# Kernel tuning notes

Measured on AMD Instinct MI355X. Metric: run time of the kernel, lower is better.

The kernel has to match this reference:

```python
import jax, jax.numpy as jnp
import numpy as np

NUM_ENT = 100000
DIM = 768
BATCH = 4096
TAU = 0.05
ALPHA = 0.5
LARGE_NUM = 1e9


def setup_inputs() -> dict:
    key = jax.random.key(0)
    k1, k2 = jax.random.split(key)
    emb = jax.random.normal(k1, (NUM_ENT, DIM), dtype=jnp.float32)
    train_links = jax.random.randint(k2, (BATCH, 2), 0, NUM_ENT, dtype=jnp.int64)
    return {"emb": emb, "train_links": train_links}


def _soft_xent(logits, batch_size):
    # target is one-hot on column i for row i -> pick diagonal of log_softmax
    logprobs = jax.nn.log_softmax(logits, axis=1)
    diag = logprobs[jnp.arange(batch_size), jnp.arange(batch_size)]
    return -jnp.sum(diag) / batch_size


def reference(emb, train_links):
    # L2-normalize embeddings (norm=True default)
    emb_n = emb / jnp.linalg.norm(emb, axis=1, keepdims=True)
    h1 = emb_n[train_links[:, 0]]  # [B, D]
    h2 = emb_n[train_links[:, 1]]  # [B, D]
    B = h1.shape[0]
    mask = jnp.eye(B, dtype=h1.dtype) * LARGE_NUM

    logits_aa = jnp.matmul(h1, h1.T) / TAU - mask  # [B, B]
    logits_bb = jnp.matmul(h2, h2.T) / TAU - mask
    logits_ab = jnp.matmul(h1, h2.T) / TAU
    logits_ba = jnp.matmul(h2, h1.T) / TAU

    logits_a = jnp.concatenate([logits_ab, logits_aa], axis=1)  # [B, 2B]
    logits_b = jnp.concatenate([logits_ba, logits_bb], axis=1)

    loss_a = _soft_xent(logits_a, B)
    loss_b = _soft_xent(logits_b, B)
    return ALPHA * loss_a + (1.0 - ALPHA) * loss_b
```

## Files before the change

### kernel.cpp

```cpp
#include <hip/hip_runtime.h>
#include <hip/hip_bf16.h>
#include <math.h>

#define NUM_ENT 100000
#define DIM 768
#define BATCH 4096
#define INV_TAU 20.0f
#define QSCALE 16.0f
#define LOGIT_SCALE (INV_TAU / (QSCALE * QSCALE))

typedef __attribute__((ext_vector_type(4))) float f32x4;

__global__ __launch_bounds__(256) void gather_norm(
    const float* __restrict__ emb, const int* __restrict__ links,
    unsigned char* __restrict__ hn1, unsigned char* __restrict__ hn2)
{
    const int t    = threadIdx.x;
    const int wave = t >> 6;
    const int lane = t & 63;
    const int rowId = blockIdx.x * 4 + wave;
    const int b     = rowId >> 1;
    const int which = rowId & 1;
    const int src   = links[2 * b + which];
    const float* srcRow = emb + (size_t)src * DIM;

    float4 v0 = ((const float4*)srcRow)[lane];
    float4 v1 = ((const float4*)srcRow)[lane + 64];
    float4 v2 = ((const float4*)srcRow)[lane + 128];

    float ss = v0.x * v0.x + v0.y * v0.y + v0.z * v0.z + v0.w * v0.w
             + v1.x * v1.x + v1.y * v1.y + v1.z * v1.z + v1.w * v1.w
             + v2.x * v2.x + v2.y * v2.y + v2.z * v2.z + v2.w * v2.w;
    #pragma unroll
    for (int off = 32; off >= 1; off >>= 1) ss += __shfl_xor(ss, off);
    const float scale = rsqrtf(ss) * QSCALE;

    unsigned char* dst = (which ? hn2 : hn1) + (size_t)b * DIM;
    int p0 = __builtin_amdgcn_cvt_pk_fp8_f32(v0.x * scale, v0.y * scale, 0, false);
    p0     = __builtin_amdgcn_cvt_pk_fp8_f32(v0.z * scale, v0.w * scale, p0, true);
    int p1 = __builtin_amdgcn_cvt_pk_fp8_f32(v1.x * scale, v1.y * scale, 0, false);
    p1     = __builtin_amdgcn_cvt_pk_fp8_f32(v1.z * scale, v1.w * scale, p1, true);
    int p2 = __builtin_amdgcn_cvt_pk_fp8_f32(v2.x * scale, v2.y * scale, 0, false);
    p2     = __builtin_amdgcn_cvt_pk_fp8_f32(v2.z * scale, v2.w * scale, p2, true);
    ((unsigned int*)dst)[lane]       = (unsigned int)p0;
    ((unsigned int*)dst)[lane + 64]  = (unsigned int)p1;
    ((unsigned int*)dst)[lane + 128] = (unsigned int)p2;
}

__global__ __launch_bounds__(256) void gram_sym(
    const unsigned char* __restrict__ hn1, const unsigned char* __restrict__ hn2,
    float* __restrict__ S, float* __restrict__ diag)
{
    const int ct = blockIdx.x;
    const int rt = blockIdx.y;
    const int matId = blockIdx.z;
    if (matId > 0 && ct < rt) return;

    const unsigned char* A  = (matId == 2) ? hn2 : hn1;
    const unsigned char* Bm = (matId == 1) ? hn1 : hn2;
    const int  rowTarget = (matId == 2) ? 1 : 0;
    const int  colTarget = (matId == 1) ? 0 : 1;
    const bool maskDiag  = (matId > 0) && (rt == ct);
    const bool doColsum  = (matId == 0) || (rt != ct);
    const bool captureDiag = (matId == 0);

    __shared__ unsigned char sA[128 * 32];
    __shared__ unsigned char sB[128 * 32];

    const int t    = threadIdx.x;
    const int lane = t & 63;
    const int wave = t >> 6;
    const int wm   = wave >> 1, wn = wave & 1;
    const int quad = lane >> 4, l16 = lane & 15;
    const int row0 = rt * 128;
    const int col0 = ct * 128;

    f32x4 acc[4][4];
    #pragma unroll
    for (int im = 0; im < 4; ++im)
        #pragma unroll
        for (int jn = 0; jn < 4; ++jn)
            acc[im][jn] = (f32x4){0.f, 0.f, 0.f, 0.f};

    for (int kk = 0; kk < DIM; kk += 32) {
        {
            int r = t >> 1, h = t & 1;
            int koff = ((h + ((r >> 2) & 1)) & 1) * 16;
            const unsigned char* ga = A  + (size_t)(row0 + r) * DIM + kk + koff;
            const unsigned char* gb = Bm + (size_t)(col0 + r) * DIM + kk + koff;
            __builtin_amdgcn_global_load_lds(
                (const __attribute__((address_space(1))) void*)ga,
                (__attribute__((address_space(3))) void*)(sA + t * 16), 16, 0, 0);
            __builtin_amdgcn_global_load_lds(
                (const __attribute__((address_space(1))) void*)gb,
                (__attribute__((address_space(3))) void*)(sB + t * 16), 16, 0, 0);
        }
        __syncthreads();

        long long af[4], bfr[4];
        const int hk = quad >> 1, q8 = (quad & 1) * 8;
        #pragma unroll
        for (int im = 0; im < 4; ++im) {
            int row = wm * 64 + im * 16 + l16;
            int hl  = (hk + ((row >> 2) & 1)) & 1;
            af[im] = *(const long long*)&sA[row * 32 + hl * 16 + q8];
        }
        #pragma unroll
        for (int jn = 0; jn < 4; ++jn) {
            int row = wn * 64 + jn * 16 + l16;
            int hl  = (hk + ((row >> 2) & 1)) & 1;
            bfr[jn] = *(const long long*)&sB[row * 32 + hl * 16 + q8];
        }

        #pragma unroll
        for (int im = 0; im < 4; ++im)
            #pragma unroll
            for (int jn = 0; jn < 4; ++jn)
                acc[im][jn] = __builtin_amdgcn_mfma_f32_16x16x32_fp8_fp8(
                    af[im], bfr[jn], acc[im][jn], 0, 0, 0);
        __syncthreads();
    }

    float csum[4] = {0.f, 0.f, 0.f, 0.f};
    #pragma unroll
    for (int im = 0; im < 4; ++im) {
        #pragma unroll
        for (int r = 0; r < 4; ++r) {
            const int gi = row0 + wm * 64 + im * 16 + quad * 4 + r;
            float rsum = 0.f;
            #pragma unroll
            for (int jn = 0; jn < 4; ++jn) {
                const int gj = col0 + wn * 64 + jn * 16 + l16;
                float logit = acc[im][jn][r] * LOGIT_SCALE;
                bool isDiag = (gi == gj);
                if (captureDiag && isDiag) diag[gi] = logit;
                float e = __expf(logit);
                if (maskDiag && isDiag) e = 0.f;
                rsum += e;
                csum[jn] += e;
            }
            rsum += __shfl_xor(rsum, 1);
            rsum += __shfl_xor(rsum, 2);
            rsum += __shfl_xor(rsum, 4);
            rsum += __shfl_xor(rsum, 8);
            if (l16 == 0) atomicAdd(&S[rowTarget * BATCH + gi], rsum);
        }
    }
    if (doColsum) {
        #pragma unroll
        for (int jn = 0; jn < 4; ++jn) {
            float c = csum[jn];
            c += __shfl_xor(c, 16);
            c += __shfl_xor(c, 32);
            if (quad == 0) {
                const int gj = col0 + wn * 64 + jn * 16 + l16;
                atomicAdd(&S[colTarget * BATCH + gj], c);
            }
        }
    }
}

__global__ __launch_bounds__(1024) void finalize(
    const float* __restrict__ S, const float* __restrict__ diag,
    float* __restrict__ out)
{
    int t = threadIdx.x;
    float local = 0.f;
    for (int i = t; i < BATCH; i += 1024) {
        float lse_a = logf(S[i]);
        float lse_b = logf(S[BATCH + i]);
        local += 0.5f * (lse_a + lse_b) - diag[i];
    }
    #pragma unroll
    for (int off = 32; off >= 1; off >>= 1) local += __shfl_xor(local, off);
    __shared__ float wsum[16];
    if ((t & 63) == 0) wsum[t >> 6] = local;
    __syncthreads();
    if (t == 0) {
        float tot = 0.f;
        #pragma unroll
        for (int w = 0; w < 16; ++w) tot += wsum[w];
        out[0] = tot / (float)BATCH;
    }
}

extern "C" void kernel_launch(void* const* d_in, const int* in_sizes, int n_in,
                              void* d_out, int out_size, void* d_ws, size_t ws_size,
                              hipStream_t stream)
{
    const float* emb  = (const float*)d_in[0];
    const int* links  = (const int*)d_in[1];

    char* ws = (char*)d_ws;
    unsigned char* hn1 = (unsigned char*)ws;
    unsigned char* hn2 = (unsigned char*)(ws + (size_t)BATCH * DIM);
    float* S    = (float*)(ws + (size_t)BATCH * DIM * 2);
    float* diag = (float*)(ws + (size_t)BATCH * DIM * 2 + 2 * BATCH * 4);

    hipMemsetAsync(S, 0, 2 * BATCH * sizeof(float), stream);

    gather_norm<<<dim3(2 * BATCH / 4), 256, 0, stream>>>(emb, links, hn1, hn2);
    gram_sym<<<dim3(32, 32, 3), 256, 0, stream>>>(hn1, hn2, S, diag);
    finalize<<<1, 1024, 0, stream>>>(S, diag, (float*)d_out);
}
```

Baseline: 426.1 us.

## Switch Gram GEMM from fp8 to int8 MFMA with 64-wide K tiles

Quantizes the normalized embeddings to int8 with scale 256 instead of fp8, and uses the 16x16x64 i8 MFMA with a 64-byte K tile and a new LDS swizzle. This halves the number of K iterations and barriers and gives better mantissa precision than fp8. It also folds the S memset into the gather kernel to drop a separate launch. Int8 clamping at 127 is safe for unit-norm rows scaled by 256 only because per-element magnitudes are small, which risks clipping outliers.

```diff
diff --git a/kernel.cpp b/kernel.cpp
--- a/kernel.cpp
+++ b/kernel.cpp
@@ -6,18 +6,30 @@
 #define DIM 768
 #define BATCH 4096
 #define INV_TAU 20.0f
-#define QSCALE 16.0f
+#define QSCALE 256.0f
 #define LOGIT_SCALE (INV_TAU / (QSCALE * QSCALE))
 
-typedef __attribute__((ext_vector_type(4))) float f32x4;
+typedef __attribute__((ext_vector_type(4))) int i32x4;
+
+__device__ inline unsigned int pack_i8x4(float a, float b, float c, float d) {
+    int ia = __float2int_rn(fminf(fmaxf(a, -127.f), 127.f));
+    int ib = __float2int_rn(fminf(fmaxf(b, -127.f), 127.f));
+    int ic = __float2int_rn(fminf(fmaxf(c, -127.f), 127.f));
+    int id = __float2int_rn(fminf(fmaxf(d, -127.f), 127.f));
+    return (unsigned int)((ia & 0xff) | ((ib & 0xff) << 8) |
+                          ((ic & 0xff) << 16) | ((id & 0xff) << 24));
+}
 
 __global__ __launch_bounds__(256) void gather_norm(
     const float* __restrict__ emb, const int* __restrict__ links,
-    unsigned char* __restrict__ hn1, unsigned char* __restrict__ hn2)
+    unsigned char* __restrict__ hn1, unsigned char* __restrict__ hn2,
+    float* __restrict__ S)
 {
     const int t    = threadIdx.x;
     const int wave = t >> 6;
     const int lane = t & 63;
+    if (blockIdx.x < 32) S[blockIdx.x * 256 + t] = 0.f;
+
     const int rowId = blockIdx.x * 4 + wave;
     const int b     = rowId >> 1;
     const int which = rowId & 1;
@@ -36,15 +48,12 @@
     const float scale = rsqrtf(ss) * QSCALE;
 
     unsigned char* dst = (which ? hn2 : hn1) + (size_t)b * DIM;
-    int p0 = __builtin_amdgcn_cvt_pk_fp8_f32(v0.x * scale, v0.y * scale, 0, false);
-    p0     = __builtin_amdgcn_cvt_pk_fp8_f32(v0.z * scale, v0.w * scale, p0, true);
-    int p1 = __builtin_amdgcn_cvt_pk_fp8_f32(v1.x * scale, v1.y * scale, 0, false);
-    p1     = __builtin_amdgcn_cvt_pk_fp8_f32(v1.z * scale, v1.w * scale, p1, true);
-    int p2 = __builtin_amdgcn_cvt_pk_fp8_f32(v2.x * scale, v2.y * scale, 0, false);
-    p2     = __builtin_amdgcn_cvt_pk_fp8_f32(v2.z * scale, v2.w * scale, p2, true);
-    ((unsigned int*)dst)[lane]       = (unsigned int)p0;
-    ((unsigned int*)dst)[lane + 64]  = (unsigned int)p1;
-    ((unsigned int*)dst)[lane + 128] = (unsigned int)p2;
+    ((unsigned int*)dst)[lane] =
+        pack_i8x4(v0.x * scale, v0.y * scale, v0.z * scale, v0.w * scale);
+    ((unsigned int*)dst)[lane + 64] =
+        pack_i8x4(v1.x * scale, v1.y * scale, v1.z * scale, v1.w * scale);
+    ((unsigned int*)dst)[lane + 128] =
+        pack_i8x4(v2.x * scale, v2.y * scale, v2.z * scale, v2.w * scale);
 }
 
 __global__ __launch_bounds__(256) void gram_sym(
@@ -64,8 +73,8 @@
     const bool doColsum  = (matId == 0) || (rt != ct);
     const bool captureDiag = (matId == 0);
 
-    __shared__ unsigned char sA[128 * 32];
-    __shared__ unsigned char sB[128 * 32];
+    __shared__ unsigned char sA[128 * 64];
+    __shared__ unsigned char sB[128 * 64];
 
     const int t    = threadIdx.x;
     const int lane = t & 63;
@@ -75,48 +84,52 @@
     const int row0 = rt * 128;
     const int col0 = ct * 128;
 
-    f32x4 acc[4][4];
+    i32x4 acc[4][4];
     #pragma unroll
     for (int im = 0; im < 4; ++im)
         #pragma unroll
         for (int jn = 0; jn < 4; ++jn)
-            acc[im][jn] = (f32x4){0.f, 0.f, 0.f, 0.f};
-
-    for (int kk = 0; kk < DIM; kk += 32) {
-        {
-            int r = t >> 1, h = t & 1;
-            int koff = ((h + ((r >> 2) & 1)) & 1) * 16;
-            const unsigned char* ga = A  + (size_t)(row0 + r) * DIM + kk + koff;
-            const unsigned char* gb = Bm + (size_t)(col0 + r) * DIM + kk + koff;
+            acc[im][jn] = (i32x4){0, 0, 0, 0};
+
+    for (int kk = 0; kk < DIM; kk += 64) {
+        #pragma unroll
+        for (int rd = 0; rd < 2; ++rd) {
+            const int idx = rd * 256 + t;
+            const int r   = idx >> 2;
+            const int p   = idx & 3;
+            const int c   = (p - (r >> 1)) & 3;
+            const unsigned char* ga = A  + (size_t)(row0 + r) * DIM + kk + c * 16;
+            const unsigned char* gb = Bm + (size_t)(col0 + r) * DIM + kk + c * 16;
             __builtin_amdgcn_global_load_lds(
                 (const __attribute__((address_space(1))) void*)ga,
-                (__attribute__((address_space(3))) void*)(sA + t * 16), 16, 0, 0);
+                (__attribute__((address_space(3))) void*)(sA + idx * 16), 16, 0, 0);
             __builtin_amdgcn_global_load_lds(
                 (const __attribute__((address_space(1))) void*)gb,
-                (__attribute__((address_space(3))) void*)(sB + t * 16), 16, 0, 0);
+                (__attribute__((address_space(3))) void*)(sB + idx * 16), 16, 0, 0);
         }
         __syncthreads();
 
-        long long af[4], bfr[4];
-        const int hk = quad >> 1, q8 = (quad & 1) * 8;
+        i32x4 af[4], bfr[4];
         #pragma unroll
         for (int im = 0; im < 4; ++im) {
             int row = wm * 64 + im * 16 + l16;
-            int hl  = (hk + ((row >> 2) & 1)) & 1;
-            af[im] = *(const long long*)&sA[row * 32 + hl * 16 + q8];
+            int p   = (quad + (row >> 1)) & 3;
+            const int4 x = *(const int4*)&sA[row * 64 + p * 16];
+            af[im] = (i32x4){x.x, x.y, x.z, x.w};
         }
         #pragma unroll
         for (int jn = 0; jn < 4; ++jn) {
             int row = wn * 64 + jn * 16 + l16;
-            int hl  = (hk + ((row >> 2) & 1)) & 1;
-            bfr[jn] = *(const long long*)&sB[row * 32 + hl * 16 + q8];
+            int p   = (quad + (row >> 1)) & 3;
+            const int4 x = *(const int4*)&sB[row * 64 + p * 16];
+            bfr[jn] = (i32x4){x.x, x.y, x.z, x.w};
         }
 
         #pragma unroll
         for (int im = 0; im < 4; ++im)
             #pragma unroll
             for (int jn = 0; jn < 4; ++jn)
-                acc[im][jn] = __builtin_amdgcn_mfma_f32_16x16x32_fp8_fp8(
+                acc[im][jn] = __builtin_amdgcn_mfma_i32_16x16x64_i8(
                     af[im], bfr[jn], acc[im][jn], 0, 0, 0);
         __syncthreads();
     }
@@ -125,13 +138,13 @@
     #pragma unroll
     for (int im = 0; im < 4; ++im) {
         #pragma unroll
-        for (int r = 0; r < 4; ++r) {
-            const int gi = row0 + wm * 64 + im * 16 + quad * 4 + r;
+        for (int rr = 0; rr < 4; ++rr) {
+            const int gi = row0 + wm * 64 + im * 16 + quad * 4 + rr;
             float rsum = 0.f;
             #pragma unroll
             for (int jn = 0; jn < 4; ++jn) {
                 const int gj = col0 + wn * 64 + jn * 16 + l16;
-                float logit = acc[im][jn][r] * LOGIT_SCALE;
+                float logit = (float)acc[im][jn][rr] * LOGIT_SCALE;
                 bool isDiag = (gi == gj);
                 if (captureDiag && isDiag) diag[gi] = logit;
                 float e = __expf(logit);
@@ -197,9 +210,7 @@
     float* S    = (float*)(ws + (size_t)BATCH * DIM * 2);
     float* diag = (float*)(ws + (size_t)BATCH * DIM * 2 + 2 * BATCH * 4);
 
-    hipMemsetAsync(S, 0, 2 * BATCH * sizeof(float), stream);
-
-    gather_norm<<<dim3(2 * BATCH / 4), 256, 0, stream>>>(emb, links, hn1, hn2);
+    gather_norm<<<dim3(2 * BATCH / 4), 256, 0, stream>>>(emb, links, hn1, hn2, S);
     gram_sym<<<dim3(32, 32, 3), 256, 0, stream>>>(hn1, hn2, S, diag);
     finalize<<<1, 1024, 0, stream>>>(S, diag, (float*)d_out);
 }
```

After: 402.5 us. -5.5%, faster.
